# Kernel optimization log

Hardware: AMD Instinct MI355X
Metric: run time of the kernel (lower is better)

## Reference

```python
import jax, jax.numpy as jnp
import numpy as np

B, C, S = 2, 3, 160  # batch, channels, cubic spatial size (in_size)


def setup_inputs() -> dict:
    key = jax.random.key(0)
    k1, k2 = jax.random.split(key)
    src = jax.random.normal(k1, (B, C, S, S, S), dtype=jnp.float32)
    flow = jax.random.normal(k2, (B, 3, S, S, S), dtype=jnp.float32)
    return {"src": src, "flow": flow, "is_msk": 0}


def _grid_sample_3d(src, z, y, x, mode):
    """F.grid_sample equivalent for 3D, align_corners=True, padding_mode='zeros'.
    z,y,x are UNNORMALIZED voxel coordinates [B,D,H,W] (the module's
    normalize-then-unnormalize with align_corners=True is an exact identity,
    so we sample at grid+flow directly -- same math, fewer round-trips)."""
    Bb, Cc, D, H, W = src.shape
    src_flat = src.reshape(Bb, Cc, D * H * W)

    def gather(iz, iy, ix):
        valid = ((iz >= 0) & (iz < D) & (iy >= 0) & (iy < H)
                 & (ix >= 0) & (ix < W))
        idx = ((jnp.clip(iz, 0, D - 1) * H + jnp.clip(iy, 0, H - 1)) * W
               + jnp.clip(ix, 0, W - 1)).reshape(Bb, 1, -1)
        v = jnp.take_along_axis(src_flat, idx, axis=2)  # [B,C,N]
        return v * valid.reshape(Bb, 1, -1).astype(src.dtype)

    if mode == 'nearest':
        # torch nearest uses round-half-to-even, same as jnp.round
        iz = jnp.round(z).astype(jnp.int32)
        iy = jnp.round(y).astype(jnp.int32)
        ix = jnp.round(x).astype(jnp.int32)
        out = gather(iz, iy, ix)
    else:  # trilinear ('bilinear')
        z0f, y0f, x0f = jnp.floor(z), jnp.floor(y), jnp.floor(x)
        tz, ty, tx = z - z0f, y - y0f, x - x0f  # fractional weights
        z0 = z0f.astype(jnp.int32); y0 = y0f.astype(jnp.int32); x0 = x0f.astype(jnp.int32)
        z1, y1, x1 = z0 + 1, y0 + 1, x0 + 1
        out = 0.
        for iz, wz in ((z0, 1. - tz), (z1, tz)):
            for iy, wy in ((y0, 1. - ty), (y1, ty)):
                for ix, wx in ((x0, 1. - tx), (x1, tx)):
                    w = (wz * wy * wx).reshape(Bb, 1, -1)
                    out = out + w * gather(iz, iy, ix)
    return out.reshape(Bb, Cc, D, H, W)


def reference(src, flow, is_msk):
    Bb, Cc, D, H, W = src.shape
    gz, gy, gx = jnp.meshgrid(jnp.arange(D, dtype=src.dtype),
                              jnp.arange(H, dtype=src.dtype),
                              jnp.arange(W, dtype=src.dtype), indexing='ij')
    # sampling location = identity grid + flow (flow channel i -> spatial axis i)
    z = gz[None] + flow[:, 0]
    y = gy[None] + flow[:, 1]
    x = gx[None] + flow[:, 2]
    mode = 'nearest' if is_msk else 'bilinear'
    return _grid_sample_3d(src, z, y, x, mode)
```

## Files before the change

### kernel.cpp

```cpp
#include <hip/hip_runtime.h>


constexpr int S  = 160;
constexpr long long S3 = (long long)S * S * S;
constexpr int BATCH = 2;
constexpr int CH = 3;

__global__ __launch_bounds__(256) void st3d_kernel(
    const float* __restrict__ src,
    const float* __restrict__ flow,
    const int*   __restrict__ is_msk,
    float*       __restrict__ out)
{
    long long tid = (long long)blockIdx.x * blockDim.x + threadIdx.x;
    if (tid >= BATCH * S3) return;
    int b = (int)(tid / S3);
    int s = (int)(tid % S3);
    int w = s % S;
    int t = s / S;
    int h = t % S;
    int d = t / S;

    const float* fb = flow + (size_t)b * 3 * S3;
    float z = (float)d + fb[s];
    float y = (float)h + fb[S3 + s];
    float x = (float)w + fb[2 * S3 + s];

    const float* sb = src + (size_t)b * CH * S3;
    float r0 = 0.f, r1 = 0.f, r2 = 0.f;

    if (__builtin_expect(*is_msk != 0, 0)) {
        int iz = (int)rintf(z), iy = (int)rintf(y), ix = (int)rintf(x);
        bool v = (unsigned)iz < (unsigned)S && (unsigned)iy < (unsigned)S &&
                 (unsigned)ix < (unsigned)S;
        int izc = min(max(iz, 0), S - 1);
        int iyc = min(max(iy, 0), S - 1);
        int ixc = min(max(ix, 0), S - 1);
        int idx = (izc * S + iyc) * S + ixc;
        float m = v ? 1.f : 0.f;
        r0 = m * sb[idx];
        r1 = m * sb[S3 + idx];
        r2 = m * sb[2 * S3 + idx];
    } else {
        float zf = floorf(z), yf = floorf(y), xf = floorf(x);
        float tz = z - zf, ty = y - yf, tx = x - xf;
        int z0 = (int)zf, y0 = (int)yf, x0 = (int)xf;
        float wz_[2] = {1.f - tz, tz};
        float wy_[2] = {1.f - ty, ty};
        float wx_[2] = {1.f - tx, tx};
        #pragma unroll
        for (int dz = 0; dz < 2; ++dz) {
            int iz = z0 + dz;
            bool vz = (unsigned)iz < (unsigned)S;
            int izc = min(max(iz, 0), S - 1);
            #pragma unroll
            for (int dy = 0; dy < 2; ++dy) {
                int iy = y0 + dy;
                bool vy = vz && ((unsigned)iy < (unsigned)S);
                int iyc = min(max(iy, 0), S - 1);
                #pragma unroll
                for (int dx = 0; dx < 2; ++dx) {
                    int ix = x0 + dx;
                    bool v = vy && ((unsigned)ix < (unsigned)S);
                    int ixc = min(max(ix, 0), S - 1);
                    int idx = (izc * S + iyc) * S + ixc;
                    float wgt = v ? wz_[dz] * wy_[dy] * wx_[dx] : 0.f;
                    r0 += wgt * sb[idx];
                    r1 += wgt * sb[S3 + idx];
                    r2 += wgt * sb[2 * S3 + idx];
                }
            }
        }
    }

    float* ob = out + (size_t)b * CH * S3;
    ob[s]          = r0;
    ob[S3 + s]     = r1;
    ob[2 * S3 + s] = r2;
}

extern "C" void kernel_launch(void* const* d_in, const int* in_sizes, int n_in,
                              void* d_out, int out_size, void* d_ws, size_t ws_size,
                              hipStream_t stream) {
    const float* src    = (const float*)d_in[0];
    const float* flow   = (const float*)d_in[1];
    const int*   is_msk = (const int*)d_in[2];
    float*       out    = (float*)d_out;

    long long total = (long long)BATCH * S3;
    int block = 256;
    int grid  = (int)((total + block - 1) / block);
    st3d_kernel<<<grid, block, 0, stream>>>(src, flow, is_msk, out);
}
```

Measured before the change: 486.4 us.

## Pair x-neighbours into 8-byte loads and swizzle blocks across XCDs

The trilinear path now fetches each x-adjacent corner pair with a single 8-byte load from a clamped base column, selecting the right element per edge case. This halves the number of gather instructions per channel. Block indices are remapped so that consecutive spatial tiles land on the same XCD, which improves L2 locality for neighbouring gathers. Index arithmetic is switched to 32-bit to drop 64-bit div/mod. The 8-byte loads may be misaligned when xl is odd, and the clamp-and-select logic adds some ALU work.

```diff
diff --git a/kernel.cpp b/kernel.cpp
--- a/kernel.cpp
+++ b/kernel.cpp
@@ -1,10 +1,14 @@
 #include <hip/hip_runtime.h>
 
 
-constexpr int S  = 160;
-constexpr long long S3 = (long long)S * S * S;
+constexpr int S   = 160;
+constexpr int S3I = S * S * S;
 constexpr int BATCH = 2;
-constexpr int CH = 3;
+constexpr int CH  = 3;
+constexpr int BLOCKS = (BATCH * S3I) / 256;
+constexpr int NXCD = 8;
+
+struct F2 { float a, b; };
 
 __global__ __launch_bounds__(256) void st3d_kernel(
     const float* __restrict__ src,
@@ -12,22 +16,23 @@
     const int*   __restrict__ is_msk,
     float*       __restrict__ out)
 {
-    long long tid = (long long)blockIdx.x * blockDim.x + threadIdx.x;
-    if (tid >= BATCH * S3) return;
-    int b = (int)(tid / S3);
-    int s = (int)(tid % S3);
+    int bid = blockIdx.x;
+    int swz = (bid % NXCD) * (BLOCKS / NXCD) + bid / NXCD;
+    int tid = swz * 256 + (int)threadIdx.x;
+    int b = tid / S3I;
+    int s = tid % S3I;
     int w = s % S;
     int t = s / S;
     int h = t % S;
     int d = t / S;
 
-    const float* fb = flow + (size_t)b * 3 * S3;
+    const float* fb = flow + (size_t)b * 3 * S3I;
     float z = (float)d + fb[s];
-    float y = (float)h + fb[S3 + s];
-    float x = (float)w + fb[2 * S3 + s];
+    float y = (float)h + fb[S3I + s];
+    float x = (float)w + fb[2 * S3I + s];
 
-    const float* sb = src + (size_t)b * CH * S3;
-    float r0 = 0.f, r1 = 0.f, r2 = 0.f;
+    const float* sb = src + (size_t)b * CH * S3I;
+    float r0, r1, r2;
 
     if (__builtin_expect(*is_msk != 0, 0)) {
         int iz = (int)rintf(z), iy = (int)rintf(y), ix = (int)rintf(x);
@@ -39,44 +44,71 @@
         int idx = (izc * S + iyc) * S + ixc;
         float m = v ? 1.f : 0.f;
         r0 = m * sb[idx];
-        r1 = m * sb[S3 + idx];
-        r2 = m * sb[2 * S3 + idx];
+        r1 = m * sb[S3I + idx];
+        r2 = m * sb[2 * S3I + idx];
     } else {
         float zf = floorf(z), yf = floorf(y), xf = floorf(x);
         float tz = z - zf, ty = y - yf, tx = x - xf;
         int z0 = (int)zf, y0 = (int)yf, x0 = (int)xf;
-        float wz_[2] = {1.f - tz, tz};
-        float wy_[2] = {1.f - ty, ty};
-        float wx_[2] = {1.f - tx, tx};
+        int z1 = z0 + 1, y1 = y0 + 1, x1 = x0 + 1;
+
+        int zc0 = min(max(z0, 0), S - 1), zc1 = min(max(z1, 0), S - 1);
+        int yc0 = min(max(y0, 0), S - 1), yc1 = min(max(y1, 0), S - 1);
+        int xl  = min(max(x0, 0), S - 2);
+
+        bool vz0 = (unsigned)z0 < (unsigned)S, vz1 = (unsigned)z1 < (unsigned)S;
+        bool vy0 = (unsigned)y0 < (unsigned)S, vy1 = (unsigned)y1 < (unsigned)S;
+        bool vx0 = (unsigned)x0 < (unsigned)S, vx1 = (unsigned)x1 < (unsigned)S;
+
+        float wz0 = 1.f - tz, wz1 = tz;
+        float wy0 = 1.f - ty, wy1 = ty;
+        float wx0 = vx0 ? (1.f - tx) : 0.f;
+        float wx1 = vx1 ? tx : 0.f;
+
+        float a00 = (vz0 && vy0) ? wz0 * wy0 : 0.f;
+        float a01 = (vz0 && vy1) ? wz0 * wy1 : 0.f;
+        float a10 = (vz1 && vy0) ? wz1 * wy0 : 0.f;
+        float a11 = (vz1 && vy1) ? wz1 * wy1 : 0.f;
+
+        int o00 = (zc0 * S + yc0) * S + xl;
+        int o01 = (zc0 * S + yc1) * S + xl;
+        int o10 = (zc1 * S + yc0) * S + xl;
+        int o11 = (zc1 * S + yc1) * S + xl;
+
+        bool sA = (x0 > xl);
+        bool sB = (x1 <= xl);
+
+        float w00A = a00 * wx0, w00B = a00 * wx1;
+        float w01A = a01 * wx0, w01B = a01 * wx1;
+        float w10A = a10 * wx0, w10B = a10 * wx1;
+        float w11A = a11 * wx0, w11B = a11 * wx1;
+
+        float racc[3];
         #pragma unroll
-        for (int dz = 0; dz < 2; ++dz) {
-            int iz = z0 + dz;
-            bool vz = (unsigned)iz < (unsigned)S;
-            int izc = min(max(iz, 0), S - 1);
-            #pragma unroll
-            for (int dy = 0; dy < 2; ++dy) {
-                int iy = y0 + dy;
-                bool vy = vz && ((unsigned)iy < (unsigned)S);
-                int iyc = min(max(iy, 0), S - 1);
-                #pragma unroll
-                for (int dx = 0; dx < 2; ++dx) {
-                    int ix = x0 + dx;
-                    bool v = vy && ((unsigned)ix < (unsigned)S);
-                    int ixc = min(max(ix, 0), S - 1);
-                    int idx = (izc * S + iyc) * S + ixc;
-                    float wgt = v ? wz_[dz] * wy_[dy] * wx_[dx] : 0.f;
-                    r0 += wgt * sb[idx];
-                    r1 += wgt * sb[S3 + idx];
-                    r2 += wgt * sb[2 * S3 + idx];
-                }
-            }
+        for (int c = 0; c < 3; ++c) {
+            const float* sc = sb + (size_t)c * S3I;
+            F2 f00 = *(const F2*)(sc + o00);
+            F2 f01 = *(const F2*)(sc + o01);
+            F2 f10 = *(const F2*)(sc + o10);
+            F2 f11 = *(const F2*)(sc + o11);
+            float v, acc;
+            v = sA ? f00.b : f00.a;  acc  = w00A * v;
+            v = sB ? f00.a : f00.b;  acc += w00B * v;
+            v = sA ? f01.b : f01.a;  acc += w01A * v;
+            v = sB ? f01.a : f01.b;  acc += w01B * v;
+            v = sA ? f10.b : f10.a;  acc += w10A * v;
+            v = sB ? f10.a : f10.b;  acc += w10B * v;
+            v = sA ? f11.b : f11.a;  acc += w11A * v;
+            v = sB ? f11.a : f11.b;  acc += w11B * v;
+            racc[c] = acc;
         }
+        r0 = racc[0]; r1 = racc[1]; r2 = racc[2];
     }
 
-    float* ob = out + (size_t)b * CH * S3;
-    ob[s]          = r0;
-    ob[S3 + s]     = r1;
-    ob[2 * S3 + s] = r2;
+    float* ob = out + (size_t)b * CH * S3I;
+    ob[s]           = r0;
+    ob[S3I + s]     = r1;
+    ob[2 * S3I + s] = r2;
 }
 
 extern "C" void kernel_launch(void* const* d_in, const int* in_sizes, int n_in,
@@ -87,8 +119,5 @@
     const int*   is_msk = (const int*)d_in[2];
     float*       out    = (float*)d_out;
 
-    long long total = (long long)BATCH * S3;
-    int block = 256;
-    int grid  = (int)((total + block - 1) / block);
-    st3d_kernel<<<grid, block, 0, stream>>>(src, flow, is_msk, out);
+    st3d_kernel<<<BLOCKS, 256, 0, stream>>>(src, flow, is_msk, out);
 }
```

New measurement: 434.8 us. 1.12x faster.
